# Kernel optimization log

Hardware: AMD Instinct MI355X
Metric: run time of the kernel (lower is better)

## Reference

```python
import jax, jax.numpy as jnp
import numpy as np


def _laplacian(x, edge_src, edge_dst, n_nodes):
    # x: [B, N, C]; L[:, i, :] = x[:, i, :] - mean over neighbors j of x[:, j, :]
    # (nodes with zero neighbors get L = 0, matching the torch loop which skips them)
    xt = jnp.transpose(x, (1, 0, 2))                      # [N, B, C]
    gathered = xt[edge_src]                               # [E, B, C]
    neigh_sum = jax.ops.segment_sum(gathered, edge_dst, num_segments=n_nodes)  # [N, B, C]
    deg = jax.ops.segment_sum(jnp.ones_like(edge_dst, dtype=x.dtype), edge_dst,
                              num_segments=n_nodes)       # [N]
    safe_deg = jnp.maximum(deg, 1.0)
    neigh_mean = neigh_sum / safe_deg[:, None, None]
    lap = jnp.where(deg[:, None, None] > 0, xt - neigh_mean, jnp.zeros((), x.dtype))
    return jnp.transpose(lap, (1, 0, 2))                  # [B, N, C]


def setup_inputs() -> dict:
    key = jax.random.key(0)
    k1, k2, k3, k4 = jax.random.split(key, 4)
    B, N, C = 4, 100000, 32
    E = 1600000  # avg degree 16
    pred = jax.random.normal(k1, (B, N, C), dtype=jnp.float32)
    target = jax.random.normal(k2, (B, N, C), dtype=jnp.float32)
    edge_src = jax.random.randint(k3, (E,), 0, N, dtype=jnp.int32)
    edge_dst = jax.random.randint(k4, (E,), 0, N, dtype=jnp.int32)
    return {"pred": pred, "target": target, "edge_src": edge_src, "edge_dst": edge_dst}


def reference(pred, target, edge_src, edge_dst):
    n_nodes = pred.shape[1]
    lap_pred = _laplacian(pred, edge_src, edge_dst, n_nodes)
    lap_target = _laplacian(target, edge_src, edge_dst, n_nodes)
    # nn.L1Loss() default reduction='mean' over all elements
    return jnp.mean(jnp.abs(lap_pred - lap_target))
```

## Files before the change

### kernel.cpp

```cpp
#include <hip/hip_runtime.h>
#include <hip/hip_bf16.h>

#define BB 4
#define CC 32

#define KMAX   512
#define STRIDE 4608

__device__ __forceinline__ unsigned pack_bf2(float x, float y) {
    unsigned bx = __float_as_uint(x); bx += 0x7fffu + ((bx >> 16) & 1u);
    unsigned by = __float_as_uint(y); by += 0x7fffu + ((by >> 16) & 1u);
    return (bx >> 16) | (by & 0xffff0000u);
}

__device__ __forceinline__ void acc_bf8(float* acc, uint4 v) {
    const unsigned* u = (const unsigned*)&v;
    #pragma unroll
    for (int k = 0; k < 4; ++k) {
        acc[2 * k]     += __uint_as_float(u[k] << 16);
        acc[2 * k + 1] += __uint_as_float(u[k] & 0xffff0000u);
    }
}

__global__ __launch_bounds__(1024) void prep_a(
        const float* __restrict__ pred, const float* __restrict__ target,
        const int* __restrict__ edge_src, const int* __restrict__ edge_dst,
        int* __restrict__ bucketCursor, unsigned* __restrict__ staged,
        unsigned* __restrict__ diffu, int N, int E, int buildBlocks, int K) {
    if ((int)blockIdx.x < buildBlocks) {
        __shared__ int cnt[KMAX];
        __shared__ int base[KMAX];
        for (int k = threadIdx.x; k < K; k += 1024) cnt[k] = 0;
        __syncthreads();
        int e0 = blockIdx.x * 8192;
        unsigned w[8]; int rp[8];
        #pragma unroll
        for (int t = 0; t < 8; ++t) {
            int i = e0 + t * 1024 + threadIdx.x;
            if (i < E) {
                int d = __builtin_nontemporal_load(&edge_dst[i]);
                int s = __builtin_nontemporal_load(&edge_src[i]);
                int bk = d >> 8;
                w[t] = (unsigned)s | ((unsigned)(d & 255) << 17);
                int r = atomicAdd(&cnt[bk], 1);
                rp[t] = r | (bk << 13);
            } else rp[t] = -1;
        }
        __syncthreads();
        for (int k = threadIdx.x; k < K; k += 1024) {
            int c = cnt[k];
            base[k] = c ? atomicAdd(&bucketCursor[k], c) : 0;
        }
        __syncthreads();
        #pragma unroll
        for (int t = 0; t < 8; ++t) {
            if (rp[t] >= 0) {
                int bk  = rp[t] >> 13;
                int pos = base[bk] + (rp[t] & 8191);
                if (pos < STRIDE)
                    staged[(size_t)bk * STRIDE + pos] = w[t];
            }
        }
    } else {
        int idx4 = ((int)blockIdx.x - buildBlocks) * 1024 + threadIdx.x;
        int total4 = N * CC;
        if (idx4 < total4) {
            int n8 = N * 8;
            int b  = idx4 / n8;
            int r  = idx4 - b * n8;
            int n  = r >> 3;
            const float4 p = *(const float4*)(pred   + ((size_t)idx4 << 2));
            const float4 t = *(const float4*)(target + ((size_t)idx4 << 2));
            uint2 u;
            u.x = pack_bf2(p.x - t.x, p.y - t.y);
            u.y = pack_bf2(p.z - t.z, p.w - t.w);
            *(uint2*)(diffu + (size_t)n * 64 + b * 16 + ((r & 7) << 1)) = u;
        }
    }
}

__global__ __launch_bounds__(256) void node_gather(
        const unsigned* __restrict__ diffu, const unsigned* __restrict__ staged,
        const int* __restrict__ bucketCursor, float* __restrict__ partials, int N) {
    __shared__ int lists[64 * 64];
    __shared__ int cnt[64];
    __shared__ float wpart[4];

    int bk  = blockIdx.x >> 2;
    int sub = blockIdx.x & 3;
    if (threadIdx.x < 64) cnt[threadIdx.x] = 0;
    __syncthreads();

    int count = min(bucketCursor[bk], STRIDE);
    const unsigned* sb = staged + (size_t)bk * STRIDE;
    for (int i = threadIdx.x; i < count; i += 256) {
        unsigned wv = sb[i];
        int loc = (wv >> 17) & 255;
        if ((loc >> 6) == sub) {
            int l = loc & 63;
            int slot = atomicAdd(&cnt[l], 1);
            if (slot < 64) lists[(l << 6) + slot] = wv & 0x1ffff;
        }
    }
    __syncthreads();

    int wave = threadIdx.x >> 6;
    int lane = threadIdx.x & 63;
    int q  = lane >> 4;
    int l4 = lane & 15;
    const unsigned* base = diffu + l4 * 4;
    int node0 = (bk << 8) + (sub << 6);
    float total = 0.0f;

    for (int t = 0; t < 16; ++t) {
        int l = (wave << 4) + t;
        int node = node0 + l;
        if (node >= N) break;
        int d = min(cnt[l], 64);
        if (d == 0) continue;
        int cs = lists[(l << 6) + lane];
        uint4 su = *(const uint4*)(base + (size_t)node * 64);

        float acc0[8], acc1[8];
        #pragma unroll
        for (int k = 0; k < 8; ++k) { acc0[k] = 0.f; acc1[k] = 0.f; }

        int j = 0;
        for (; j + 15 < d; j += 16) {
            int sA = __shfl(cs, j + q, 64);
            int sB = __shfl(cs, j + 4 + q, 64);
            int sC = __shfl(cs, j + 8 + q, 64);
            int sD = __shfl(cs, j + 12 + q, 64);
            uint4 vA = *(const uint4*)(base + (size_t)sA * 64);
            uint4 vB = *(const uint4*)(base + (size_t)sB * 64);
            uint4 vC = *(const uint4*)(base + (size_t)sC * 64);
            uint4 vD = *(const uint4*)(base + (size_t)sD * 64);
            acc_bf8(acc0, vA); acc_bf8(acc1, vB);
            acc_bf8(acc0, vC); acc_bf8(acc1, vD);
        }
        for (; j + 3 < d; j += 4) {
            int sA = __shfl(cs, j + q, 64);
            uint4 vA = *(const uint4*)(base + (size_t)sA * 64);
            acc_bf8(acc0, vA);
        }
        if (j < d) {
            int idx = j + q;
            int sA = __shfl(cs, idx < d ? idx : 0, 64);
            if (idx < d) {
                uint4 vA = *(const uint4*)(base + (size_t)sA * 64);
                acc_bf8(acc1, vA);
            }
        }
        float inv = 1.0f / (float)d;
        const unsigned* sp = (const unsigned*)&su;
        #pragma unroll
        for (int k = 0; k < 8; ++k) {
            float v = acc0[k] + acc1[k];
            v += __shfl_down(v, 32, 64);
            v += __shfl_down(v, 16, 64);
            if (lane < 16) {
                unsigned spk = sp[k >> 1];
                float s = (k & 1) ? __uint_as_float(spk & 0xffff0000u)
                                  : __uint_as_float(spk << 16);
                total += fabsf(s - v * inv);
            }
        }
    }
    #pragma unroll
    for (int delta = 8; delta >= 1; delta >>= 1)
        total += __shfl_down(total, delta, 64);
    if (lane == 0) wpart[wave] = total;
    __syncthreads();
    if (threadIdx.x == 0)
        partials[blockIdx.x] = wpart[0] + wpart[1] + wpart[2] + wpart[3];
}

__global__ __launch_bounds__(256) void reduce_kernel(const float* __restrict__ partials, int n,
                                                     float* __restrict__ out, float inv_count) {
    float s = 0.0f;
    for (int i = threadIdx.x; i < n; i += 256) s += partials[i];
    int lane = threadIdx.x & 63;
    int wave = threadIdx.x >> 6;
    #pragma unroll
    for (int delta = 32; delta >= 1; delta >>= 1)
        s += __shfl_down(s, delta, 64);
    __shared__ float wpart[4];
    if (lane == 0) wpart[wave] = s;
    __syncthreads();
    if (threadIdx.x == 0)
        out[0] = (wpart[0] + wpart[1] + wpart[2] + wpart[3]) * inv_count;
}

__global__ void build_kernel(const int* __restrict__ edge_src, const int* __restrict__ edge_dst,
                             int* __restrict__ deg, int* __restrict__ csr, int E) {
    int i = blockIdx.x * 256 + threadIdx.x;
    if (i < E) {
        int d = edge_dst[i];
        int slot = atomicAdd(&deg[d], 1);
        if (slot < 64) csr[(d << 6) + slot] = edge_src[i];
    }
}

__global__ __launch_bounds__(256) void node_kernel_pt(const float* __restrict__ pred,
                                                      const float* __restrict__ target,
                                                      const int* __restrict__ csr,
                                                      const int* __restrict__ deg,
                                                      float* __restrict__ partials, int N) {
    int wave = threadIdx.x >> 6;
    int lane = threadIdx.x & 63;
    int node = blockIdx.x * 4 + wave;
    float total = 0.0f;
    if (node < N) {
        int d = min(deg[node], 64);
        if (d > 0) {
            int o = node << 6;
            int cs = csr[o + lane];
            int b = (lane >> 3) & 3;
            int q = lane & 7;
            const float* arr = (lane >= 32) ? target : pred;
            int rowbase = b * N * CC + q * 4;
            float4 sp = *(const float4*)(pred + rowbase + node * CC);
            float4 st = *(const float4*)(target + rowbase + node * CC);
            float ax = 0.f, ay = 0.f, az = 0.f, aw = 0.f;
            for (int j = 0; j < d; ++j) {
                int s = __shfl(cs, j, 64);
                float4 v = *(const float4*)(arr + rowbase + s * CC);
                ax += v.x; ay += v.y; az += v.z; aw += v.w;
            }
            float dx = ax - __shfl_down(ax, 32, 64);
            float dy = ay - __shfl_down(ay, 32, 64);
            float dz = az - __shfl_down(az, 32, 64);
            float dw = aw - __shfl_down(aw, 32, 64);
            if (lane < 32) {
                float inv = 1.0f / (float)d;
                total = fabsf((sp.x - st.x) - dx * inv)
                      + fabsf((sp.y - st.y) - dy * inv)
                      + fabsf((sp.z - st.z) - dz * inv)
                      + fabsf((sp.w - st.w) - dw * inv);
            }
        }
    }
    #pragma unroll
    for (int delta = 32; delta >= 1; delta >>= 1)
        total += __shfl_down(total, delta, 64);
    __shared__ float wpart[4];
    if (lane == 0) wpart[wave] = total;
    __syncthreads();
    if (threadIdx.x == 0)
        partials[blockIdx.x] = wpart[0] + wpart[1] + wpart[2] + wpart[3];
}

extern "C" void kernel_launch(void* const* d_in, const int* in_sizes, int n_in,
                              void* d_out, int out_size, void* d_ws, size_t ws_size,
                              hipStream_t stream) {
    const float* pred   = (const float*)d_in[0];
    const float* target = (const float*)d_in[1];
    const int* edge_src = (const int*)d_in[2];
    const int* edge_dst = (const int*)d_in[3];
    float* out = (float*)d_out;

    const int BNC = in_sizes[0];
    const int E   = in_sizes[2];
    const int N   = BNC / (BB * CC);
    const int K   = (N + 255) >> 8;

    size_t staged_off = 512;
    size_t diff_off   = staged_off + (size_t)K * STRIDE;
    diff_off = (diff_off + 3) & ~(size_t)3;
    size_t part_off   = diff_off + ((size_t)N << 6);
    size_t fast_bytes = (part_off + (size_t)4 * K + 16) * 4;

    if (ws_size >= fast_bytes && N <= 131072 && K <= KMAX) {
        int* cursor = (int*)d_ws;
        unsigned* staged = (unsigned*)((int*)d_ws + staged_off);
        unsigned* diffu = (unsigned*)((int*)d_ws + diff_off);
        float* partials = (float*)((int*)d_ws + part_off);

        hipMemsetAsync(cursor, 0, 512 * sizeof(int), stream);
        const int buildBlocks = (E + 8191) / 8192;
        const int diffBlocks  = (N * CC + 1023) / 1024;
        prep_a<<<buildBlocks + diffBlocks, 1024, 0, stream>>>(
            pred, target, edge_src, edge_dst, cursor, staged, diffu,
            N, E, buildBlocks, K);
        node_gather<<<4 * K, 256, 0, stream>>>(diffu, staged, cursor, partials, N);
        reduce_kernel<<<1, 256, 0, stream>>>(partials, 4 * K, out, 1.0f / (float)BNC);
    } else {
        int* deg = (int*)d_ws;
        int* csr = deg + N;
        float* partials = (float*)(csr + ((size_t)N << 6));
        const int nblocks4 = (N + 3) / 4;

        hipMemsetAsync(deg, 0, (size_t)N * sizeof(int), stream);
        const int eblocks = (E + 255) / 256;
        build_kernel<<<eblocks, 256, 0, stream>>>(edge_src, edge_dst, deg, csr, E);
        node_kernel_pt<<<nblocks4, 256, 0, stream>>>(pred, target, csr, deg, partials, N);
        reduce_kernel<<<1, 256, 0, stream>>>(partials, nblocks4, out, 1.0f / (float)BNC);
    }
}
```

Baseline: 211.4 us.

## Fuse final reduction via atomics, widen gather blocks, use packed float adds

Removes the separate reduce kernel. Each node_gather block now atomically adds its scaled partial straight into the output, which prep_a zeroes first. node_gather moves to 512 threads, so 8 waves each handle 8 nodes, and block IDs are remapped to interleave buckets and sub-blocks. Accumulation uses 2-wide float vectors so the compiler can emit packed adds, and the pred/target loads in prep_a become nontemporal. The float atomic sum makes the result order-dependent, and the larger blocks change occupancy.

```diff
diff --git a/kernel.cpp b/kernel.cpp
--- a/kernel.cpp
+++ b/kernel.cpp
@@ -6,6 +6,9 @@
 
 #define KMAX   512
 #define STRIDE 4608
+
+typedef float v2f __attribute__((ext_vector_type(2)));
+typedef float v4f __attribute__((ext_vector_type(4)));
 
 __device__ __forceinline__ unsigned pack_bf2(float x, float y) {
     unsigned bx = __float_as_uint(x); bx += 0x7fffu + ((bx >> 16) & 1u);
@@ -13,12 +16,14 @@
     return (bx >> 16) | (by & 0xffff0000u);
 }
 
-__device__ __forceinline__ void acc_bf8(float* acc, uint4 v) {
+__device__ __forceinline__ void acc_bf8(v2f* acc, uint4 v) {
     const unsigned* u = (const unsigned*)&v;
     #pragma unroll
     for (int k = 0; k < 4; ++k) {
-        acc[2 * k]     += __uint_as_float(u[k] << 16);
-        acc[2 * k + 1] += __uint_as_float(u[k] & 0xffff0000u);
+        v2f t;
+        t.x = __uint_as_float(u[k] << 16);
+        t.y = __uint_as_float(u[k] & 0xffff0000u);
+        acc[k] += t;
     }
 }
 
@@ -26,7 +31,9 @@
         const float* __restrict__ pred, const float* __restrict__ target,
         const int* __restrict__ edge_src, const int* __restrict__ edge_dst,
         int* __restrict__ bucketCursor, unsigned* __restrict__ staged,
-        unsigned* __restrict__ diffu, int N, int E, int buildBlocks, int K) {
+        unsigned* __restrict__ diffu, float* __restrict__ outz,
+        int N, int E, int buildBlocks, int K) {
+    if (blockIdx.x == 0 && threadIdx.x == 0) *outz = 0.0f;
     if ((int)blockIdx.x < buildBlocks) {
         __shared__ int cnt[KMAX];
         __shared__ int base[KMAX];
@@ -69,8 +76,8 @@
             int b  = idx4 / n8;
             int r  = idx4 - b * n8;
             int n  = r >> 3;
-            const float4 p = *(const float4*)(pred   + ((size_t)idx4 << 2));
-            const float4 t = *(const float4*)(target + ((size_t)idx4 << 2));
+            const v4f p = __builtin_nontemporal_load((const v4f*)pred + idx4);
+            const v4f t = __builtin_nontemporal_load((const v4f*)target + idx4);
             uint2 u;
             u.x = pack_bf2(p.x - t.x, p.y - t.y);
             u.y = pack_bf2(p.z - t.z, p.w - t.w);
@@ -79,21 +86,33 @@
     }
 }
 
-__global__ __launch_bounds__(256) void node_gather(
+__global__ __launch_bounds__(512) void node_gather(
         const unsigned* __restrict__ diffu, const unsigned* __restrict__ staged,
-        const int* __restrict__ bucketCursor, float* __restrict__ partials, int N) {
+        const int* __restrict__ bucketCursor, float* __restrict__ out,
+        int N, int K, float inv_count) {
     __shared__ int lists[64 * 64];
     __shared__ int cnt[64];
-    __shared__ float wpart[4];
-
-    int bk  = blockIdx.x >> 2;
-    int sub = blockIdx.x & 3;
+    __shared__ float wpart[8];
+
+    int bid = (int)blockIdx.x;
+    int bk, sub;
+    int full = (K >> 3) << 5;
+    if (bid < full) {
+        int chunk = bid >> 5, r = bid & 31;
+        bk  = (chunk << 3) + (r & 7);
+        sub = r >> 3;
+    } else {
+        int r = bid - full;
+        bk  = (K & ~7) + (r >> 2);
+        sub = r & 3;
+    }
+
     if (threadIdx.x < 64) cnt[threadIdx.x] = 0;
     __syncthreads();
 
     int count = min(bucketCursor[bk], STRIDE);
     const unsigned* sb = staged + (size_t)bk * STRIDE;
-    for (int i = threadIdx.x; i < count; i += 256) {
+    for (int i = threadIdx.x; i < count; i += 512) {
         unsigned wv = sb[i];
         int loc = (wv >> 17) & 255;
         if ((loc >> 6) == sub) {
@@ -112,8 +131,8 @@
     int node0 = (bk << 8) + (sub << 6);
     float total = 0.0f;
 
-    for (int t = 0; t < 16; ++t) {
-        int l = (wave << 4) + t;
+    for (int t = 0; t < 8; ++t) {
+        int l = (wave << 3) + t;
         int node = node0 + l;
         if (node >= N) break;
         int d = min(cnt[l], 64);
@@ -121,9 +140,10 @@
         int cs = lists[(l << 6) + lane];
         uint4 su = *(const uint4*)(base + (size_t)node * 64);
 
-        float acc0[8], acc1[8];
-        #pragma unroll
-        for (int k = 0; k < 8; ++k) { acc0[k] = 0.f; acc1[k] = 0.f; }
+        v2f zero; zero.x = 0.0f; zero.y = 0.0f;
+        v2f acc0[4], acc1[4];
+        #pragma unroll
+        for (int k = 0; k < 4; ++k) { acc0[k] = zero; acc1[k] = zero; }
 
         int j = 0;
         for (; j + 15 < d; j += 16) {
@@ -154,15 +174,17 @@
         float inv = 1.0f / (float)d;
         const unsigned* sp = (const unsigned*)&su;
         #pragma unroll
-        for (int k = 0; k < 8; ++k) {
-            float v = acc0[k] + acc1[k];
-            v += __shfl_down(v, 32, 64);
-            v += __shfl_down(v, 16, 64);
+        for (int k = 0; k < 4; ++k) {
+            v2f v = acc0[k] + acc1[k];
+            float vx = v.x, vy = v.y;
+            vx += __shfl_down(vx, 32, 64);
+            vx += __shfl_down(vx, 16, 64);
+            vy += __shfl_down(vy, 32, 64);
+            vy += __shfl_down(vy, 16, 64);
             if (lane < 16) {
-                unsigned spk = sp[k >> 1];
-                float s = (k & 1) ? __uint_as_float(spk & 0xffff0000u)
-                                  : __uint_as_float(spk << 16);
-                total += fabsf(s - v * inv);
+                unsigned spk = sp[k];
+                total += fabsf(__uint_as_float(spk << 16)         - vx * inv)
+                       + fabsf(__uint_as_float(spk & 0xffff0000u) - vy * inv);
             }
         }
     }
@@ -171,8 +193,12 @@
         total += __shfl_down(total, delta, 64);
     if (lane == 0) wpart[wave] = total;
     __syncthreads();
-    if (threadIdx.x == 0)
-        partials[blockIdx.x] = wpart[0] + wpart[1] + wpart[2] + wpart[3];
+    if (threadIdx.x == 0) {
+        float s = 0.0f;
+        #pragma unroll
+        for (int w = 0; w < 8; ++w) s += wpart[w];
+        atomicAdd(out, s * inv_count);
+    }
 }
 
 __global__ __launch_bounds__(256) void reduce_kernel(const float* __restrict__ partials, int n,
@@ -267,23 +293,21 @@
     size_t staged_off = 512;
     size_t diff_off   = staged_off + (size_t)K * STRIDE;
     diff_off = (diff_off + 3) & ~(size_t)3;
-    size_t part_off   = diff_off + ((size_t)N << 6);
-    size_t fast_bytes = (part_off + (size_t)4 * K + 16) * 4;
+    size_t fast_bytes = (diff_off + ((size_t)N << 6) + 16) * 4;
 
     if (ws_size >= fast_bytes && N <= 131072 && K <= KMAX) {
         int* cursor = (int*)d_ws;
         unsigned* staged = (unsigned*)((int*)d_ws + staged_off);
         unsigned* diffu = (unsigned*)((int*)d_ws + diff_off);
-        float* partials = (float*)((int*)d_ws + part_off);
 
         hipMemsetAsync(cursor, 0, 512 * sizeof(int), stream);
         const int buildBlocks = (E + 8191) / 8192;
         const int diffBlocks  = (N * CC + 1023) / 1024;
         prep_a<<<buildBlocks + diffBlocks, 1024, 0, stream>>>(
-            pred, target, edge_src, edge_dst, cursor, staged, diffu,
+            pred, target, edge_src, edge_dst, cursor, staged, diffu, out,
             N, E, buildBlocks, K);
-        node_gather<<<4 * K, 256, 0, stream>>>(diffu, staged, cursor, partials, N);
-        reduce_kernel<<<1, 256, 0, stream>>>(partials, 4 * K, out, 1.0f / (float)BNC);
+        node_gather<<<4 * K, 512, 0, stream>>>(diffu, staged, cursor, out, N, K,
+                                               1.0f / (float)BNC);
     } else {
         int* deg = (int*)d_ws;
         int* csr = deg + N;
```

After: 214.7 us. No clear change (+1.6%).
